# Kernel tuning notes

Hardware: AMD Instinct MI355X
Metric: run time of the kernel (lower is better)

## Reference

```python
import jax, jax.numpy as jnp
import numpy as np

PATCH = 2      # patch_size
NQ = 4         # n_qubits (state vector has 2**NQ amplitudes)
NL = 2         # n_layers
IMG = 28
NB = IMG // PATCH          # 14 patch blocks per side
NP = NB * NB               # 196 patches


def _bc(c, ndim):
    # broadcast a (B,P) or scalar coefficient against the remaining wire axes
    return c.reshape(c.shape + (1,) * (ndim - c.ndim)) if jnp.ndim(c) else c


def _apply_ry(state, theta, w):
    # state: (B, P, 2,2,2,2); theta: scalar or (B, P)
    st = jnp.moveaxis(state, 2 + w, -1)
    s0, s1 = st[..., 0], st[..., 1]
    h = theta * 0.5
    c = _bc(jnp.cos(h), s0.ndim)
    s = _bc(jnp.sin(h), s0.ndim)
    st = jnp.stack([c * s0 - s * s1, s * s0 + c * s1], axis=-1)
    return jnp.moveaxis(st, -1, 2 + w)


def _apply_rz(state, theta, w):
    st = jnp.moveaxis(state, 2 + w, -1)
    ph = _bc(jnp.exp(-0.5j * theta), st[..., 0].ndim)  # e^{-i theta/2}
    st = jnp.stack([ph * st[..., 0], jnp.conj(ph) * st[..., 1]], axis=-1)
    return jnp.moveaxis(st, -1, 2 + w)


def _apply_cnot(state, cw, tw):
    # control wire cw, target wire tw (cw < tw)
    st = jnp.moveaxis(state, (2 + cw, 2 + tw), (-2, -1))
    c0 = st[..., 0, :]
    c1 = jnp.stack([st[..., 1, 1], st[..., 1, 0]], axis=-1)  # flip target when control=1
    st = jnp.stack([c0, c1], axis=-2)
    return jnp.moveaxis(st, (-2, -1), (2 + cw, 2 + tw))


def _simulate(angles, var_params):
    # angles: (B, NP, NQ) encoder RY angles (pixel values); var_params: (NL, 2, NQ)
    B, P, _ = angles.shape
    state = jnp.zeros((B, P, 2 ** NQ), jnp.complex64).at[:, :, 0].set(1.0)
    state = state.reshape((B, P) + (2,) * NQ)
    for w in range(NQ):                       # GeneralEncoder: RY(x_i) on wire i
        state = _apply_ry(state, angles[:, :, w], w)
    for l in range(NL):                       # variational layers
        for w in range(NQ):
            state = _apply_ry(state, var_params[l, 0, w], w)
        for w in range(NQ):
            state = _apply_rz(state, var_params[l, 1, w], w)
        for c in range(NQ - 1):               # CNOT entanglement chain
            state = _apply_cnot(state, c, c + 1)
    probs = state.real ** 2 + state.imag ** 2  # (B, P, 2,2,2,2)
    exps = []
    for w in range(NQ):                        # <Z_w> = P(bit_w=0) - P(bit_w=1)
        other = tuple(2 + k for k in range(NQ) if k != w)
        p = probs.sum(axis=other)              # (B, P, 2)
        exps.append(p[..., 0] - p[..., 1])
    return jnp.stack(exps, axis=-1)            # (B, P, NQ)


def setup_inputs() -> dict:
    key = jax.random.key(0)
    k1, k2, k3 = jax.random.split(key, 3)
    B = 2048
    x = jax.random.uniform(k1, (B, IMG, IMG), dtype=jnp.float32)
    var_params = jax.random.normal(k2, (NL, 2, NQ), dtype=jnp.float32)
    W = jax.random.normal(k3, (10, NP * NQ), dtype=jnp.float32) * 0.03
    b = jnp.zeros((10,), dtype=jnp.float32)
    return {"x": x, "var_params": var_params, "W": W, "b": b}


def reference(x, var_params, W, b):
    B = x.shape[0]
    # extract non-overlapping PATCHxPATCH patches, row-major within patch
    patches = x.reshape(B, NB, PATCH, NB, PATCH).transpose(0, 1, 3, 2, 4)
    patches = patches.reshape(B, NP, PATCH * PATCH)
    meas = _simulate(patches, var_params)      # (B, NP, NQ)
    feats = meas.reshape(B, NP * NQ)           # patch-major concat, matches torch.cat
    logits = feats @ W.T + b
    return jax.nn.log_softmax(logits, axis=-1)
```

## Files before the change

### kernel.cpp

```cpp
#include <hip/hip_runtime.h>
#include <math.h>

#define NCLS 10


__global__ __launch_bounds__(256)
void quanv_fused(const float* __restrict__ x, const float* __restrict__ vp,
                 const float* __restrict__ W, const float* __restrict__ bias,
                 float* __restrict__ out) {
    __shared__ float K[30];
    __shared__ float4 feats4[196];
    __shared__ float logitsS[NCLS];

    const int b = blockIdx.x;
    const int t = threadIdx.x;

    if (t == 224) {
        float c1[4], s1[4], fx[4], fy[4];
        #pragma unroll
        for (int w = 0; w < 4; ++w) {
            __sincosf(vp[8 + w], &s1[w], &c1[w]);
            __sincosf(vp[4 + w], &fy[w], &fx[w]);
        }
        K[0] = c1[0];
        K[1] = -s1[0] * fx[0] * fx[1];
        K[2] =  c1[0] * c1[1];
        K[3] = -c1[0] * s1[1] * fx[1] * fx[2];
        K[4] =  s1[0] * c1[1] * fy[0] * fy[1];
        K[5] =  s1[0] * s1[1] * fx[0] * fx[2];
        K[6]  =  c1[0] * c1[1] * c1[2];
        K[7]  = -c1[0] * c1[1] * s1[2] * fx[2] * fx[3];
        K[8]  =  c1[0] * s1[1] * c1[2] * fy[1] * fy[2];
        K[9]  =  c1[0] * s1[1] * s1[2] * fx[1] * fx[3];
        K[10] = -s1[0] * c1[1] * c1[2] * fx[0] * fx[1];
        K[11] = -s1[0] * c1[1] * s1[2] * fy[0] * fy[1] * fx[2] * fx[3];
        K[12] = -s1[0] * s1[1] * c1[2] * fy[0] * fy[2];
        K[13] = -s1[0] * s1[1] * s1[2] * fx[0] * fx[3];
        K[14] =  c1[0] * c1[1] * c1[2] * c1[3];
        K[15] = -c1[0] * c1[1] * c1[2] * s1[3] * fx[3];
        K[16] =  c1[0] * c1[1] * s1[2] * c1[3] * fy[2] * fy[3];
        K[17] =  c1[0] * c1[1] * s1[2] * s1[3] * fx[2];
        K[18] = -c1[0] * s1[1] * c1[2] * c1[3] * fx[1] * fx[2];
        K[19] = -c1[0] * s1[1] * c1[2] * s1[3] * fy[1] * fy[2] * fx[3];
        K[20] = -c1[0] * s1[1] * s1[2] * c1[3] * fy[1] * fy[3];
        K[21] = -c1[0] * s1[1] * s1[2] * s1[3] * fx[1];
        K[22] =  s1[0] * c1[1] * c1[2] * c1[3] * fy[0] * fy[1];
        K[23] =  s1[0] * c1[1] * c1[2] * s1[3] * fx[0] * fx[1] * fx[3];
        K[24] = -s1[0] * c1[1] * s1[2] * c1[3] * fx[0] * fx[1] * fy[2] * fy[3];
        K[25] =  s1[0] * c1[1] * s1[2] * s1[3] * fy[0] * fy[1] * fx[2];
        K[26] =  s1[0] * s1[1] * c1[2] * c1[3] * fx[0] * fx[2];
        K[27] =  s1[0] * s1[1] * c1[2] * s1[3] * fy[0] * fy[2] * fx[3];
        K[28] =  s1[0] * s1[1] * s1[2] * c1[3] * fy[0] * fy[3];
        K[29] =  s1[0] * s1[1] * s1[2] * s1[3] * fx[0];
    }

    const bool is_sim = (t < 196);
    float cA[4], sA[4];
    if (is_sim) {
        const int i = t / 14;
        const int j = t - i * 14;
        const float* xb = x + b * 784 + 2 * i * 28 + 2 * j;
        const float2 A  = *(const float2*)xb;
        const float2 Bv = *(const float2*)(xb + 28);
        __sincosf(A.x  + vp[0], &sA[0], &cA[0]);
        __sincosf(A.y  + vp[1], &sA[1], &cA[1]);
        __sincosf(Bv.x + vp[2], &sA[2], &cA[2]);
        __sincosf(Bv.y + vp[3], &sA[3], &cA[3]);
    }
    __syncthreads();

    if (is_sim) {
        const float s01 = sA[0] * sA[1];
        const float s23 = sA[2] * sA[3];
        const float e0 = K[0] * cA[0] + K[1] * s01;
        const float e1 = K[2] * cA[1] + K[3] * (cA[0] * sA[1] * sA[2])
                       + K[4] * s01   + K[5] * (sA[0] * sA[2]);
        const float e2 = K[6]  * (cA[0] * cA[2])
                       + K[7]  * (cA[1] * s23)
                       + K[8]  * (sA[1] * sA[2])
                       + K[9]  * (cA[0] * sA[1] * sA[3])
                       + K[10] * (s01 * cA[2])
                       + K[11] * (s01 * s23)
                       + K[12] * (sA[0] * cA[1] * sA[2])
                       + K[13] * (sA[0] * sA[3]);
        const float e3 = K[14] * (cA[1] * cA[3])
                       + K[15] * (cA[0] * cA[2] * sA[3])
                       + K[16] * (cA[0] * s23)
                       + K[17] * (cA[1] * sA[2])
                       + K[18] * (cA[0] * sA[1] * sA[2] * cA[3])
                       + K[19] * (sA[1] * s23)
                       + K[20] * (sA[1] * cA[2] * sA[3])
                       + K[21] * (cA[0] * sA[1])
                       + K[22] * (s01 * cA[3])
                       + K[23] * (s01 * cA[2] * sA[3])
                       + K[24] * (s01 * s23)
                       + K[25] * (s01 * sA[2])
                       + K[26] * (sA[0] * sA[2] * cA[3])
                       + K[27] * (sA[0] * cA[1] * sA[2] * sA[3])
                       + K[28] * (sA[0] * cA[1] * cA[2] * sA[3])
                       + K[29] * sA[0];
        feats4[t] = make_float4(e0, e1, e2, e3);
    }
    __syncthreads();

    const int c = t >> 4, j = t & 15;
    float acc = 0.0f;
    if (c < NCLS) {
        const float4* __restrict__ W4 = (const float4*)W;
        #pragma unroll
        for (int i2 = 0; i2 < 12; ++i2) {
            const int v = j + 16 * i2;
            const float4 f = feats4[v];
            const float4 w = W4[c * 196 + v];
            acc += f.x * w.x + f.y * w.y + f.z * w.z + f.w * w.w;
        }
        if (j < 4) {
            const int v = j + 192;
            const float4 f = feats4[v];
            const float4 w = W4[c * 196 + v];
            acc += f.x * w.x + f.y * w.y + f.z * w.z + f.w * w.w;
        }
    }
    acc += __shfl_down(acc, 8, 16);
    acc += __shfl_down(acc, 4, 16);
    acc += __shfl_down(acc, 2, 16);
    acc += __shfl_down(acc, 1, 16);
    if (j == 0 && c < NCLS) logitsS[c] = acc + bias[c];
    __syncthreads();

    if (t < NCLS) {
        float m = -1e30f;
        #pragma unroll
        for (int k = 0; k < NCLS; ++k) m = fmaxf(m, logitsS[k]);
        float ssum = 0.0f;
        #pragma unroll
        for (int k = 0; k < NCLS; ++k) ssum += __expf(logitsS[k] - m);
        out[b * NCLS + t] = logitsS[t] - m - __logf(ssum);
    }
}

extern "C" void kernel_launch(void* const* d_in, const int* in_sizes, int n_in,
                              void* d_out, int out_size, void* d_ws, size_t ws_size,
                              hipStream_t stream) {
    const float* x  = (const float*)d_in[0];
    const float* vp = (const float*)d_in[1];
    const float* W  = (const float*)d_in[2];
    const float* bb = (const float*)d_in[3];
    float* out = (float*)d_out;

    quanv_fused<<<2048, 256, 0, stream>>>(x, vp, W, bb, out);
}
```

Before: 67.19 us.

## Map one wavefront per image and remove shared memory and block barriers

Restructures the kernel so each 64-lane wavefront processes a whole image. Each lane loops over up to four patches and accumulates all ten class logits in registers. The cross-lane reduction uses wave shuffles, and the log-softmax is computed redundantly in every lane. Every thread now computes the variational constants itself instead of one thread writing them to shared memory. This removes all __syncthreads and the idle threads from the per-image layout, at the cost of more registers, redundant sincos per thread, and 60 wave-level shuffle reductions.

```diff
diff --git a/kernel.cpp b/kernel.cpp
--- a/kernel.cpp
+++ b/kernel.cpp
@@ -8,14 +8,12 @@
 void quanv_fused(const float* __restrict__ x, const float* __restrict__ vp,
                  const float* __restrict__ W, const float* __restrict__ bias,
                  float* __restrict__ out) {
-    __shared__ float K[30];
-    __shared__ float4 feats4[196];
-    __shared__ float logitsS[NCLS];
+    const int l   = threadIdx.x & 63;
+    const int wv  = threadIdx.x >> 6;
+    const int img = blockIdx.x * 4 + wv;
 
-    const int b = blockIdx.x;
-    const int t = threadIdx.x;
-
-    if (t == 224) {
+    float K[30];
+    {
         float c1[4], s1[4], fx[4], fy[4];
         #pragma unroll
         for (int w = 0; w < 4; ++w) {
@@ -53,90 +51,91 @@
         K[28] =  s1[0] * s1[1] * s1[2] * c1[3] * fy[0] * fy[3];
         K[29] =  s1[0] * s1[1] * s1[2] * s1[3] * fx[0];
     }
+    const float v0 = vp[0], v1 = vp[1], v2 = vp[2], v3 = vp[3];
 
-    const bool is_sim = (t < 196);
-    float cA[4], sA[4];
-    if (is_sim) {
-        const int i = t / 14;
-        const int j = t - i * 14;
-        const float* xb = x + b * 784 + 2 * i * 28 + 2 * j;
-        const float2 A  = *(const float2*)xb;
-        const float2 Bv = *(const float2*)(xb + 28);
-        __sincosf(A.x  + vp[0], &sA[0], &cA[0]);
-        __sincosf(A.y  + vp[1], &sA[1], &cA[1]);
-        __sincosf(Bv.x + vp[2], &sA[2], &cA[2]);
-        __sincosf(Bv.y + vp[3], &sA[3], &cA[3]);
-    }
-    __syncthreads();
+    float acc[NCLS];
+    #pragma unroll
+    for (int c = 0; c < NCLS; ++c) acc[c] = 0.0f;
 
-    if (is_sim) {
-        const float s01 = sA[0] * sA[1];
-        const float s23 = sA[2] * sA[3];
-        const float e0 = K[0] * cA[0] + K[1] * s01;
-        const float e1 = K[2] * cA[1] + K[3] * (cA[0] * sA[1] * sA[2])
-                       + K[4] * s01   + K[5] * (sA[0] * sA[2]);
-        const float e2 = K[6]  * (cA[0] * cA[2])
-                       + K[7]  * (cA[1] * s23)
-                       + K[8]  * (sA[1] * sA[2])
-                       + K[9]  * (cA[0] * sA[1] * sA[3])
-                       + K[10] * (s01 * cA[2])
-                       + K[11] * (s01 * s23)
-                       + K[12] * (sA[0] * cA[1] * sA[2])
-                       + K[13] * (sA[0] * sA[3]);
-        const float e3 = K[14] * (cA[1] * cA[3])
-                       + K[15] * (cA[0] * cA[2] * sA[3])
-                       + K[16] * (cA[0] * s23)
-                       + K[17] * (cA[1] * sA[2])
-                       + K[18] * (cA[0] * sA[1] * sA[2] * cA[3])
-                       + K[19] * (sA[1] * s23)
-                       + K[20] * (sA[1] * cA[2] * sA[3])
-                       + K[21] * (cA[0] * sA[1])
-                       + K[22] * (s01 * cA[3])
-                       + K[23] * (s01 * cA[2] * sA[3])
-                       + K[24] * (s01 * s23)
-                       + K[25] * (s01 * sA[2])
-                       + K[26] * (sA[0] * sA[2] * cA[3])
-                       + K[27] * (sA[0] * cA[1] * sA[2] * sA[3])
-                       + K[28] * (sA[0] * cA[1] * cA[2] * sA[3])
-                       + K[29] * sA[0];
-        feats4[t] = make_float4(e0, e1, e2, e3);
-    }
-    __syncthreads();
+    const float4* __restrict__ W4 = (const float4*)W;
+    const float* __restrict__ xb0 = x + img * 784;
 
-    const int c = t >> 4, j = t & 15;
-    float acc = 0.0f;
-    if (c < NCLS) {
-        const float4* __restrict__ W4 = (const float4*)W;
-        #pragma unroll
-        for (int i2 = 0; i2 < 12; ++i2) {
-            const int v = j + 16 * i2;
-            const float4 f = feats4[v];
-            const float4 w = W4[c * 196 + v];
-            acc += f.x * w.x + f.y * w.y + f.z * w.z + f.w * w.w;
-        }
-        if (j < 4) {
-            const int v = j + 192;
-            const float4 f = feats4[v];
-            const float4 w = W4[c * 196 + v];
-            acc += f.x * w.x + f.y * w.y + f.z * w.z + f.w * w.w;
+    #pragma unroll
+    for (int r = 0; r < 4; ++r) {
+        const int p = l + 64 * r;
+        if (r < 3 || l < 4) {
+            const int i = p / 14;
+            const int j = p - i * 14;
+            const float* xb = xb0 + i * 56 + 2 * j;
+            const float2 A  = *(const float2*)xb;
+            const float2 Bv = *(const float2*)(xb + 28);
+
+            float cA[4], sA[4];
+            __sincosf(A.x  + v0, &sA[0], &cA[0]);
+            __sincosf(A.y  + v1, &sA[1], &cA[1]);
+            __sincosf(Bv.x + v2, &sA[2], &cA[2]);
+            __sincosf(Bv.y + v3, &sA[3], &cA[3]);
+
+            const float s01 = sA[0] * sA[1];
+            const float s23 = sA[2] * sA[3];
+            const float e0 = K[0] * cA[0] + K[1] * s01;
+            const float e1 = K[2] * cA[1] + K[3] * (cA[0] * sA[1] * sA[2])
+                           + K[4] * s01   + K[5] * (sA[0] * sA[2]);
+            const float e2 = K[6]  * (cA[0] * cA[2])
+                           + K[7]  * (cA[1] * s23)
+                           + K[8]  * (sA[1] * sA[2])
+                           + K[9]  * (cA[0] * sA[1] * sA[3])
+                           + K[10] * (s01 * cA[2])
+                           + K[11] * (s01 * s23)
+                           + K[12] * (sA[0] * cA[1] * sA[2])
+                           + K[13] * (sA[0] * sA[3]);
+            const float e3 = K[14] * (cA[1] * cA[3])
+                           + K[15] * (cA[0] * cA[2] * sA[3])
+                           + K[16] * (cA[0] * s23)
+                           + K[17] * (cA[1] * sA[2])
+                           + K[18] * (cA[0] * sA[1] * sA[2] * cA[3])
+                           + K[19] * (sA[1] * s23)
+                           + K[20] * (sA[1] * cA[2] * sA[3])
+                           + K[21] * (cA[0] * sA[1])
+                           + K[22] * (s01 * cA[3])
+                           + K[23] * (s01 * cA[2] * sA[3])
+                           + K[24] * (s01 * s23)
+                           + K[25] * (s01 * sA[2])
+                           + K[26] * (sA[0] * sA[2] * cA[3])
+                           + K[27] * (sA[0] * cA[1] * sA[2] * sA[3])
+                           + K[28] * (sA[0] * cA[1] * cA[2] * sA[3])
+                           + K[29] * sA[0];
+
+            #pragma unroll
+            for (int c = 0; c < NCLS; ++c) {
+                const float4 w = W4[c * 196 + p];
+                acc[c] += e0 * w.x + e1 * w.y + e2 * w.z + e3 * w.w;
+            }
         }
     }
-    acc += __shfl_down(acc, 8, 16);
-    acc += __shfl_down(acc, 4, 16);
-    acc += __shfl_down(acc, 2, 16);
-    acc += __shfl_down(acc, 1, 16);
-    if (j == 0 && c < NCLS) logitsS[c] = acc + bias[c];
-    __syncthreads();
 
-    if (t < NCLS) {
-        float m = -1e30f;
-        #pragma unroll
-        for (int k = 0; k < NCLS; ++k) m = fmaxf(m, logitsS[k]);
-        float ssum = 0.0f;
-        #pragma unroll
-        for (int k = 0; k < NCLS; ++k) ssum += __expf(logitsS[k] - m);
-        out[b * NCLS + t] = logitsS[t] - m - __logf(ssum);
+    #pragma unroll
+    for (int c = 0; c < NCLS; ++c) {
+        float v = acc[c];
+        v += __shfl_xor(v, 1);
+        v += __shfl_xor(v, 2);
+        v += __shfl_xor(v, 4);
+        v += __shfl_xor(v, 8);
+        v += __shfl_xor(v, 16);
+        v += __shfl_xor(v, 32);
+        acc[c] = v + bias[c];
     }
+
+    float m = acc[0];
+    #pragma unroll
+    for (int c = 1; c < NCLS; ++c) m = fmaxf(m, acc[c]);
+    float ssum = 0.0f;
+    #pragma unroll
+    for (int c = 0; c < NCLS; ++c) ssum += __expf(acc[c] - m);
+    const float lse = m + __logf(ssum);
+    #pragma unroll
+    for (int c = 0; c < NCLS; ++c)
+        if (l == c) out[img * NCLS + c] = acc[c] - lse;
 }
 
 extern "C" void kernel_launch(void* const* d_in, const int* in_sizes, int n_in,
@@ -148,5 +147,5 @@
     const float* bb = (const float*)d_in[3];
     float* out = (float*)d_out;
 
-    quanv_fused<<<2048, 256, 0, stream>>>(x, vp, W, bb, out);
+    quanv_fused<<<512, 256, 0, stream>>>(x, vp, W, bb, out);
 }
```

New measurement: 67.36 us. About the same (+0.2%).
